# Kernel tuning notes

Hardware: AMD Instinct MI355X
Metric: run time of the kernel (lower is better)

The kernel has to match this reference:

```python
import jax, jax.numpy as jnp
import numpy as np

N = 10000          # nodes
E_RAND = 320000    # random edges (avg degree 32)
F_IN = 512         # nfeat
HID = 256          # args.hid
HEADS = 8          # args.head
FH = HID // HEADS  # 32 per head
NCLASS = 40
TAU = 0.5
LAMDA = 0.5
K = 2


def setup_inputs() -> dict:
    key = jax.random.key(0)
    ks = jax.random.split(key, 16)
    # edge list: random edges + self-loops (so every dst segment is non-empty)
    src = jnp.concatenate([jax.random.randint(ks[0], (E_RAND,), 0, N), jnp.arange(N)])
    dst = jnp.concatenate([jax.random.randint(ks[1], (E_RAND,), 0, N), jnp.arange(N)])
    s = 0.05  # small init scale keeps exp() in attention/bind_loss stable
    return {
        "x": jax.random.normal(ks[2], (N, F_IN), jnp.float32),
        "src": src, "dst": dst,
        "W0": jax.random.normal(ks[3], (F_IN, HEADS, FH), jnp.float32) * s,
        "a0s": jax.random.normal(ks[4], (HEADS, FH), jnp.float32) * s,
        "a0d": jax.random.normal(ks[5], (HEADS, FH), jnp.float32) * s,
        "W1": jax.random.normal(ks[6], (HID, HEADS, FH), jnp.float32) * s,
        "a1s": jax.random.normal(ks[7], (HEADS, FH), jnp.float32) * s,
        "a1d": jax.random.normal(ks[8], (HEADS, FH), jnp.float32) * s,
        "W2": jax.random.normal(ks[9], (HID, HEADS, FH), jnp.float32) * s,
        "a2s": jax.random.normal(ks[10], (HEADS, FH), jnp.float32) * s,
        "a2d": jax.random.normal(ks[11], (HEADS, FH), jnp.float32) * s,
        "Wout": jax.random.normal(ks[12], (HID, HEADS, NCLASS), jnp.float32) * s,
        "aos": jax.random.normal(ks[13], (HEADS, NCLASS), jnp.float32) * s,
        "aod": jax.random.normal(ks[14], (HEADS, NCLASS), jnp.float32) * s,
    }


def _gat_layer(x, W, a_s, a_d, src, dst):
    """Sparse multi-head GAT layer: gather -> edge softmax -> scatter."""
    n = x.shape[0]
    h = jnp.einsum('nf,fhd->nhd', x, W)              # [N,H,Fh]
    es = jnp.sum(h * a_s, axis=-1)                    # [N,H]
    ed = jnp.sum(h * a_d, axis=-1)                    # [N,H]
    e = jax.nn.leaky_relu(es[src] + ed[dst], 0.2)     # [E,H]
    m = jax.ops.segment_max(e, dst, num_segments=n)   # per-dst max (stable softmax)
    w = jnp.exp(e - m[dst])
    z = jax.ops.segment_sum(w, dst, num_segments=n)
    alpha = w / z[dst]                                # [E,H]
    return jax.ops.segment_sum(alpha[:, :, None] * h[src], dst, num_segments=n)  # [N,H,Fh]


def _bind_loss(z):
    # z1 == z2 == z in the original call site: refl_sim == between_sim
    zn = z / jnp.maximum(jnp.linalg.norm(z, axis=1, keepdims=True), 1e-12)
    S = jnp.exp(jnp.matmul(zn, zn.T) / TAU)           # [N,N]
    d = jnp.diagonal(S)
    off = jnp.sum(S, axis=1) - d                      # masked (off-diagonal) row sum
    CT = -jnp.log(d / (off + off))                    # neg_c2.sum + neg_c3.sum
    return jnp.mean(CT)


def reference(x, src, dst, W0, a0s, a0d, W1, a1s, a1d, W2, a2s, a2d, Wout, aos, aod):
    layers = [(W0, a0s, a0d), (W1, a1s, a1d), (W2, a2s, a2d)]
    last = x
    loss = jnp.float32(0.0)
    for i, (W, as_, ad_) in enumerate(layers):
        cur = jax.nn.elu(_gat_layer(last, W, as_, ad_, src, dst))
        cur = cur.reshape(cur.shape[0], -1)           # concat heads -> [N, HID]
        if i > 0:
            beta = LAMDA / (i + 2)                    # MaskLayer(last, cur, lamda, i+2)
            cur = beta * last + (1.0 - beta) * cur
            if i % K == 0:
                loss = loss + _bind_loss(cur)
        last = cur
    out = _gat_layer(last, Wout, aos, aod, src, dst).mean(axis=1)  # avg heads -> [N,C]
    return (jax.nn.log_softmax(out, axis=1), loss)
```

## Files before the change

### kernel.cpp

```cpp
#include <hip/hip_runtime.h>
#include <hip/hip_bf16.h>
#include <math.h>

#define NN_F_IN   512
#define NN_HID    256
#define NN_HEADS  8
#define NN_FH     32
#define NN_NCLASS 40
#define TAU_F     0.5f
#define LAMDA_F   0.5f

typedef __attribute__((ext_vector_type(8))) short bf16x8;
typedef __attribute__((ext_vector_type(4))) float f32x4;

static __device__ __forceinline__ float lrelu02(float x) { return x >= 0.f ? x : 0.2f * x; }
static __device__ __forceinline__ float elu1(float x)    { return x > 0.f ? x : expm1f(x); }
static __device__ __forceinline__ float b2f(unsigned short u) {
    unsigned int x = ((unsigned int)u) << 16;
    return __uint_as_float(x);
}
static __device__ __forceinline__ unsigned short f2b(float f) {
    __hip_bfloat16 hb = __float2bfloat16(f);
    return *reinterpret_cast<unsigned short*>(&hb);
}

__global__ void prep_kernel(const float* __restrict__ x,
                            const float* __restrict__ W0, const float* __restrict__ W1,
                            const float* __restrict__ W2, const float* __restrict__ Wo,
                            unsigned short* __restrict__ Xb,
                            unsigned short* __restrict__ Wt0, unsigned short* __restrict__ Wt1,
                            unsigned short* __restrict__ Wt2, unsigned short* __restrict__ Wto,
                            int n4X) {
    int i = blockIdx.x * 256 + threadIdx.x;
    if (i < n4X) {
        float4 v = *(const float4*)(x + (size_t)i * 4);
        ushort4 o;
        o.x = f2b(v.x); o.y = f2b(v.y); o.z = f2b(v.z); o.w = f2b(v.w);
        *(ushort4*)(Xb + (size_t)i * 4) = o;
        return;
    }
    i -= n4X;
    if (i < 256 * 512) {
        int np = i >> 9, k = i & 511;
        Wt0[i] = f2b(W0[(size_t)k * 256 + np]);
        return;
    }
    i -= 256 * 512;
    if (i < 256 * 256) {
        int np = i >> 8, k = i & 255;
        Wt1[i] = f2b(W1[(size_t)k * 256 + np]);
        return;
    }
    i -= 256 * 256;
    if (i < 256 * 256) {
        int np = i >> 8, k = i & 255;
        Wt2[i] = f2b(W2[(size_t)k * 256 + np]);
        return;
    }
    i -= 256 * 256;
    if (i < 384 * 256) {
        int np = i >> 8, k = i & 255;
        Wto[i] = f2b(np < 320 ? Wo[(size_t)k * 320 + np] : 0.f);
    }
}

__global__ __launch_bounds__(256) void fc_mfma(const unsigned short* __restrict__ A,
                                               const unsigned short* __restrict__ B,
                                               unsigned short* __restrict__ H,
                                               int M, int K, int ncols, int ldH) {
    int t = threadIdx.x, lane = t & 63, wid = t >> 6;
    int wrow = wid >> 1, wcol = wid & 1;
    int l15 = lane & 15, lg = lane >> 4;
    int mbase = blockIdx.y * 64 + wrow * 32;
    int nbase = blockIdx.x * 64 + wcol * 32;

    const unsigned short* Ap[2];
    const unsigned short* Bp[2];
#pragma unroll
    for (int m = 0; m < 2; ++m) {
        int rr = mbase + m * 16 + l15;
        if (rr > M - 1) rr = M - 1;
        Ap[m] = A + (size_t)rr * K + lg * 8;
        Bp[m] = B + (size_t)(nbase + m * 16 + l15) * K + lg * 8;
    }
    f32x4 acc[2][2];
#pragma unroll
    for (int m = 0; m < 2; ++m)
#pragma unroll
        for (int nn = 0; nn < 2; ++nn)
#pragma unroll
            for (int r = 0; r < 4; ++r) acc[m][nn][r] = 0.f;

    bf16x8 aP[2], bP[2], aQ[2], bQ[2];
#pragma unroll
    for (int m = 0; m < 2; ++m) {
        aP[m] = *(const bf16x8*)(Ap[m]);
        bP[m] = *(const bf16x8*)(Bp[m]);
    }
    int nhalf = K >> 6;
    int kk = 32;
    for (int it = 0; it < nhalf; ++it) {
#pragma unroll
        for (int m = 0; m < 2; ++m) {
            aQ[m] = *(const bf16x8*)(Ap[m] + kk);
            bQ[m] = *(const bf16x8*)(Bp[m] + kk);
        }
#pragma unroll
        for (int m = 0; m < 2; ++m)
#pragma unroll
            for (int nn = 0; nn < 2; ++nn)
                acc[m][nn] = __builtin_amdgcn_mfma_f32_16x16x32_bf16(aP[m], bP[nn], acc[m][nn], 0, 0, 0);
        if (it + 1 < nhalf) {
#pragma unroll
            for (int m = 0; m < 2; ++m) {
                aP[m] = *(const bf16x8*)(Ap[m] + kk + 32);
                bP[m] = *(const bf16x8*)(Bp[m] + kk + 32);
            }
        }
#pragma unroll
        for (int m = 0; m < 2; ++m)
#pragma unroll
            for (int nn = 0; nn < 2; ++nn)
                acc[m][nn] = __builtin_amdgcn_mfma_f32_16x16x32_bf16(aQ[m], bQ[nn], acc[m][nn], 0, 0, 0);
        kk += 64;
    }
#pragma unroll
    for (int m = 0; m < 2; ++m) {
#pragma unroll
        for (int nn = 0; nn < 2; ++nn) {
            int col = nbase + nn * 16 + l15;
            if (col >= ncols) continue;
#pragma unroll
            for (int r = 0; r < 4; ++r) {
                int row = mbase + m * 16 + lg * 4 + r;
                if (row < M) H[(size_t)row * ldH + col] = f2b(acc[m][nn][r]);
            }
        }
    }
}

__global__ void attn_kernel(const unsigned short* __restrict__ Hm, const float* __restrict__ As,
                            const float* __restrict__ Ad, float* __restrict__ es,
                            float* __restrict__ ed, int n, int df) {
    int idx = blockIdx.x * blockDim.x + threadIdx.x;
    if (idx >= n * NN_HEADS) return;
    int nn = idx / NN_HEADS, hh = idx - nn * NN_HEADS;
    const unsigned short* hp = Hm + (size_t)nn * NN_HEADS * df + hh * df;
    const float* ap = As + hh * df;
    const float* bp = Ad + hh * df;
    float s1 = 0.f, s2 = 0.f;
    for (int d = 0; d < df; d += 4) {
        ushort4 hv = *(const ushort4*)(hp + d);
        float4 av = *(const float4*)(ap + d);
        float4 bv = *(const float4*)(bp + d);
        float h0 = b2f(hv.x), h1 = b2f(hv.y), h2 = b2f(hv.z), h3 = b2f(hv.w);
        s1 += h0 * av.x + h1 * av.y + h2 * av.z + h3 * av.w;
        s2 += h0 * bv.x + h1 * bv.y + h2 * bv.z + h3 * bv.w;
    }
    es[idx] = s1;
    ed[idx] = s2;
}

__global__ __launch_bounds__(256) void edge_wz(
    const float* __restrict__ es, const float* __restrict__ ed,
    const int* __restrict__ csr_src, const int* __restrict__ row_start,
    float* __restrict__ wC, float* __restrict__ zinv, int n) {
    int lane = threadIdx.x & 63;
    int nn   = blockIdx.x * 4 + (threadIdx.x >> 6);
    if (nn >= n) return;
    int s0 = row_start[nn], s1 = row_start[nn + 1];
    int h    = lane & 7;
    int slot = lane >> 3;
    float edh = ed[nn * NN_HEADS + h];
    float z = 0.f;
    for (int e = s0 + slot; e < s1; e += 8) {
        int sv = csr_src[e];
        float w = __expf(lrelu02(es[sv * NN_HEADS + h] + edh));
        wC[(size_t)e * NN_HEADS + h] = w;
        z += w;
    }
    z += __shfl_xor(z, 8, 64);
    z += __shfl_xor(z, 16, 64);
    z += __shfl_xor(z, 32, 64);
    if (slot == 0) zinv[nn * NN_HEADS + h] = 1.f / z;
}

__global__ void count_kernel(const int* __restrict__ dst, int* __restrict__ counts, int E) {
    int e = blockIdx.x * blockDim.x + threadIdx.x;
    if (e < E) atomicAdd(&counts[dst[e]], 1);
}

__global__ void scan_kernel(const int* __restrict__ counts, int* __restrict__ row_start,
                            int* __restrict__ cursor, int n) {
    __shared__ int s[1024];
    int t  = threadIdx.x;
    int ch = (n + 1023) / 1024;
    int lo = t * ch;
    int sum = 0;
    for (int j = 0; j < ch; ++j) {
        int i = lo + j;
        if (i < n) sum += counts[i];
    }
    s[t] = sum;
    __syncthreads();
    for (int off = 1; off < 1024; off <<= 1) {
        int v = 0;
        if (t >= off) v = s[t - off];
        __syncthreads();
        s[t] += v;
        __syncthreads();
    }
    int run = (t == 0) ? 0 : s[t - 1];
    for (int j = 0; j < ch; ++j) {
        int i = lo + j;
        if (i < n) {
            row_start[i] = run;
            cursor[i] = run;
            run += counts[i];
        }
    }
    if (t == 1023) row_start[n] = s[1023];
}

__global__ void scatter_kernel(const int* __restrict__ src, const int* __restrict__ dst,
                               int* __restrict__ cursor, int* __restrict__ csr_src, int E) {
    int e = blockIdx.x * blockDim.x + threadIdx.x;
    if (e < E) {
        int d   = dst[e];
        int pos = atomicAdd(&cursor[d], 1);
        csr_src[pos] = src[e];
    }
}

__global__ __launch_bounds__(256) void gather_hidden(
    const unsigned short* __restrict__ Hm, const float* __restrict__ wC,
    const float* __restrict__ zinv, const int* __restrict__ csr_src,
    const int* __restrict__ row_start, const unsigned short* __restrict__ last,
    unsigned short* __restrict__ out, int n, float beta) {
    int lane = threadIdx.x & 63;
    int nn   = blockIdx.x * 4 + (threadIdx.x >> 6);
    if (nn >= n) return;
    int s0 = row_start[nn], s1 = row_start[nn + 1];
    int h2 = lane >> 3;

    float a0 = 0.f, a1 = 0.f, a2 = 0.f, a3 = 0.f;
    int fullEnd = s0 + ((s1 - s0) & ~7);
    int e = s0;
    for (; e < fullEnd; e += 8) {
        int idx[8];
        float wv[8];
#pragma unroll
        for (int j = 0; j < 8; ++j) {
            idx[j] = csr_src[e + j];
            wv[j]  = wC[(size_t)(e + j) * NN_HEADS + h2];
        }
        ushort4 r[8];
#pragma unroll
        for (int j = 0; j < 8; ++j) r[j] = *(const ushort4*)&Hm[(size_t)idx[j] * NN_HID + lane * 4];
#pragma unroll
        for (int j = 0; j < 8; ++j) {
            float w = wv[j];
            a0 += w * b2f(r[j].x); a1 += w * b2f(r[j].y);
            a2 += w * b2f(r[j].z); a3 += w * b2f(r[j].w);
        }
    }
    if (e < s1) {
        int c = s1 - e;
        int idx[8];
        float wv[8];
#pragma unroll
        for (int j = 0; j < 8; ++j) {
            int p = (j < c) ? e + j : e;
            idx[j] = csr_src[p];
            wv[j]  = wC[(size_t)p * NN_HEADS + h2];
        }
        ushort4 r[8];
#pragma unroll
        for (int j = 0; j < 8; ++j) r[j] = *(const ushort4*)&Hm[(size_t)idx[j] * NN_HID + lane * 4];
#pragma unroll
        for (int j = 0; j < 8; ++j) {
            if (j < c) {
                float w = wv[j];
                a0 += w * b2f(r[j].x); a1 += w * b2f(r[j].y);
                a2 += w * b2f(r[j].z); a3 += w * b2f(r[j].w);
            }
        }
    }
    float zi = zinv[nn * NN_HEADS + h2];
    float v0 = elu1(a0 * zi), v1 = elu1(a1 * zi), v2 = elu1(a2 * zi), v3 = elu1(a3 * zi);
    if (beta >= 0.f) {
        ushort4 lv = *(const ushort4*)&last[(size_t)nn * NN_HID + lane * 4];
        v0 = beta * b2f(lv.x) + (1.f - beta) * v0;
        v1 = beta * b2f(lv.y) + (1.f - beta) * v1;
        v2 = beta * b2f(lv.z) + (1.f - beta) * v2;
        v3 = beta * b2f(lv.w) + (1.f - beta) * v3;
    }
    ushort4 o;
    o.x = f2b(v0); o.y = f2b(v1); o.z = f2b(v2); o.w = f2b(v3);
    *(ushort4*)&out[(size_t)nn * NN_HID + lane * 4] = o;
}

__global__ void gather_final(const unsigned short* __restrict__ Hm, const float* __restrict__ wC,
                             const float* __restrict__ zinv, const int* __restrict__ csr_src,
                             const int* __restrict__ row_start, float* __restrict__ dout, int n) {
    int nn = blockIdx.x;
    __shared__ float accs[NN_HEADS * NN_NCLASS];
    int t = threadIdx.x;
    int s0 = row_start[nn], s1 = row_start[nn + 1];
    int hh = t / NN_NCLASS;
    float acc = 0.f;
    const int LD = NN_HEADS * NN_NCLASS;
    int fullEnd = s0 + ((s1 - s0) & ~7);
    int e = s0;
    for (; e < fullEnd; e += 8) {
        int idx[8];
        float wv[8];
#pragma unroll
        for (int j = 0; j < 8; ++j) {
            idx[j] = csr_src[e + j];
            wv[j]  = wC[(size_t)(e + j) * NN_HEADS + hh];
        }
        float v[8];
#pragma unroll
        for (int j = 0; j < 8; ++j) v[j] = b2f(Hm[(size_t)idx[j] * LD + t]);
#pragma unroll
        for (int j = 0; j < 8; ++j) acc += wv[j] * v[j];
    }
    if (e < s1) {
        int c = s1 - e;
        int idx[8];
        float wv[8];
#pragma unroll
        for (int j = 0; j < 8; ++j) {
            int p = (j < c) ? e + j : e;
            idx[j] = csr_src[p];
            wv[j]  = wC[(size_t)p * NN_HEADS + hh];
        }
        float v[8];
#pragma unroll
        for (int j = 0; j < 8; ++j) v[j] = b2f(Hm[(size_t)idx[j] * LD + t]);
#pragma unroll
        for (int j = 0; j < 8; ++j) {
            if (j < c) acc += wv[j] * v[j];
        }
    }
    accs[t] = acc * zinv[nn * NN_HEADS + hh];
    __syncthreads();
    if (t < 64) {
        float v = -INFINITY;
        if (t < NN_NCLASS) {
            float sacc = 0.f;
#pragma unroll
            for (int h2 = 0; h2 < NN_HEADS; ++h2) sacc += accs[h2 * NN_NCLASS + t];
            v = sacc * (1.f / NN_HEADS);
        }
        float mx = v;
#pragma unroll
        for (int o = 1; o < 64; o <<= 1) mx = fmaxf(mx, __shfl_xor(mx, o, 64));
        float ex = (t < NN_NCLASS) ? expf(v - mx) : 0.f;
        float se = ex;
#pragma unroll
        for (int o = 1; o < 64; o <<= 1) se += __shfl_xor(se, o, 64);
        if (t < NN_NCLASS) dout[(size_t)nn * NN_NCLASS + t] = (v - mx) - logf(se);
    }
}

__global__ void rownorm_kernel(const unsigned short* __restrict__ z, short* __restrict__ znb,
                               float* __restrict__ dvec, int n) {
    int nn = blockIdx.x;
    int t  = threadIdx.x;
    float v  = b2f(z[(size_t)nn * NN_HID + t]);
    float sq = v * v;
#pragma unroll
    for (int o = 1; o < 64; o <<= 1) sq += __shfl_xor(sq, o, 64);
    __shared__ float ws[4];
    if ((t & 63) == 0) ws[t >> 6] = sq;
    __syncthreads();
    float s = ws[0] + ws[1] + ws[2] + ws[3];
    float m = fmaxf(sqrtf(s), 1e-12f);
    znb[(size_t)nn * NN_HID + t] = (short)f2b(v / m);
    if (t == 0) dvec[nn] = __expf((s / (m * m)) * (1.f / TAU_F));
}

__global__ __launch_bounds__(256) void gram_mfma(const short* __restrict__ znb,
                                                 float* __restrict__ P2d, int n,
                                                 int T, int nwg, int Npad) {
    __shared__ short As[2][128 * 64];
    __shared__ short Bs[2][128 * 64];

    int b = blockIdx.x;
    int q = nwg >> 3, r8 = nwg & 7, xc = b & 7, oo = b >> 3;
    int sid = (xc < r8 ? xc * (q + 1) : r8 * (q + 1) + (xc - r8) * q) + oo;
    int bi = 0, rem = sid;
    while (rem >= T - bi) { rem -= T - bi; ++bi; }
    int bj = bi + rem;
    int i0 = bi * 128, j0 = bj * 128;

    int t    = threadIdx.x;
    int lane = t & 63;
    int wid  = t >> 6;
    int wrow = wid >> 1, wcol = wid & 1;
    int l15  = lane & 15, lg = lane >> 4;
    int srow = lane >> 3;
    int sch  = lane & 7;

    f32x4 acc[4][4];
#pragma unroll
    for (int m = 0; m < 4; ++m)
#pragma unroll
        for (int nn = 0; nn < 4; ++nn)
#pragma unroll
            for (int r = 0; r < 4; ++r) acc[m][nn][r] = 0.f;

    bf16x8 sa[2][4], sb[2][4];
#pragma unroll
    for (int sl = 0; sl < 2; ++sl)
#pragma unroll
        for (int s = 0; s < 4; ++s) {
            int row = wid * 32 + s * 8 + srow;
            int gch = sch ^ (row & 7);
            sa[sl][s] = *(const bf16x8*)(znb + (size_t)(i0 + row) * NN_HID + sl * 64 + gch * 8);
            sb[sl][s] = *(const bf16x8*)(znb + (size_t)(j0 + row) * NN_HID + sl * 64 + gch * 8);
        }

#pragma unroll
    for (int kt = 0; kt < 2; ++kt) {
#pragma unroll
        for (int sl = 0; sl < 2; ++sl)
#pragma unroll
            for (int s = 0; s < 4; ++s) {
                int row = wid * 32 + s * 8 + srow;
                *(bf16x8*)(&As[sl][row * 64 + sch * 8]) = sa[sl][s];
                *(bf16x8*)(&Bs[sl][row * 64 + sch * 8]) = sb[sl][s];
            }
        __syncthreads();
        if (kt == 0) {
#pragma unroll
            for (int sl = 0; sl < 2; ++sl)
#pragma unroll
                for (int s = 0; s < 4; ++s) {
                    int row = wid * 32 + s * 8 + srow;
                    int gch = sch ^ (row & 7);
                    sa[sl][s] = *(const bf16x8*)(znb + (size_t)(i0 + row) * NN_HID + 128 + sl * 64 + gch * 8);
                    sb[sl][s] = *(const bf16x8*)(znb + (size_t)(j0 + row) * NN_HID + 128 + sl * 64 + gch * 8);
                }
        }
#pragma unroll
        for (int sl = 0; sl < 2; ++sl) {
#pragma unroll
            for (int ks = 0; ks < 2; ++ks) {
                bf16x8 av[4], bv[4];
#pragma unroll
                for (int m = 0; m < 4; ++m) {
                    int Ra = wrow * 64 + m * 16 + l15;
                    int Rb = wcol * 64 + m * 16 + l15;
                    int ca = (ks * 4 + lg) ^ (Ra & 7);
                    int cb = (ks * 4 + lg) ^ (Rb & 7);
                    av[m] = *(const bf16x8*)(&As[sl][Ra * 64 + ca * 8]);
                    bv[m] = *(const bf16x8*)(&Bs[sl][Rb * 64 + cb * 8]);
                }
#pragma unroll
                for (int m = 0; m < 4; ++m)
#pragma unroll
                    for (int nn = 0; nn < 4; ++nn)
                        acc[m][nn] = __builtin_amdgcn_mfma_f32_16x16x32_bf16(av[m], bv[nn], acc[m][nn], 0, 0, 0);
            }
        }
        if (kt == 0) __syncthreads();
    }

    int i0w = i0 + wrow * 64;
    int j0w = j0 + wcol * 64;
    bool diag = (bj == bi);
#pragma unroll
    for (int m = 0; m < 4; ++m)
#pragma unroll
        for (int nn = 0; nn < 4; ++nn) {
            int gj = j0w + nn * 16 + l15;
            bool jok = gj < n;
#pragma unroll
            for (int r = 0; r < 4; ++r) {
                int gi = i0w + m * 16 + lg * 4 + r;
                acc[m][nn][r] = (jok && gi < n) ? __expf(acc[m][nn][r] * (1.f / TAU_F)) : 0.f;
            }
        }
    float* rowslot = P2d + (size_t)(2 * bj + wcol) * Npad;
#pragma unroll
    for (int m = 0; m < 4; ++m) {
#pragma unroll
        for (int r = 0; r < 4; ++r) {
            float v = acc[m][0][r] + acc[m][1][r] + acc[m][2][r] + acc[m][3][r];
            v += __shfl_xor(v, 1, 64);
            v += __shfl_xor(v, 2, 64);
            v += __shfl_xor(v, 4, 64);
            v += __shfl_xor(v, 8, 64);
            if (l15 == 0) {
                int gi = i0w + m * 16 + lg * 4 + r;
                if (gi < n) rowslot[gi] = v;
            }
        }
    }
    if (!diag) {
        float* colslot = P2d + (size_t)(2 * bi + wrow) * Npad;
#pragma unroll
        for (int nn = 0; nn < 4; ++nn) {
            float v = 0.f;
#pragma unroll
            for (int m = 0; m < 4; ++m)
#pragma unroll
                for (int r = 0; r < 4; ++r) v += acc[m][nn][r];
            v += __shfl_xor(v, 16, 64);
            v += __shfl_xor(v, 32, 64);
            if (lg == 0) {
                int gj = j0w + nn * 16 + l15;
                if (gj < n) colslot[gj] = v;
            }
        }
    }
}

__global__ void fold_kernel(const float* __restrict__ P2d, float* __restrict__ R,
                            int n, int slots, int Npad) {
    int i = blockIdx.x * 256 + threadIdx.x;
    if (i >= n) return;
    const float* p = P2d + i;
    float s0 = 0.f, s1 = 0.f, s2 = 0.f, s3 = 0.f;
    int sl = 0;
    for (; sl + 4 <= slots; sl += 4) {
        s0 += p[(size_t)(sl + 0) * Npad];
        s1 += p[(size_t)(sl + 1) * Npad];
        s2 += p[(size_t)(sl + 2) * Npad];
        s3 += p[(size_t)(sl + 3) * Npad];
    }
    for (; sl < slots; ++sl) s0 += p[(size_t)sl * Npad];
    R[i] = (s0 + s1) + (s2 + s3);
}

__global__ void loss_kernel(const float* __restrict__ R, const float* __restrict__ dvec,
                            float* __restrict__ out_loss, int n) {
    __shared__ float s[1024];
    int t = threadIdx.x;
    float sum = 0.f;
    for (int i = t; i < n; i += 1024) {
        float d   = dvec[i];
        float off = R[i] - d;
        sum += -logf(d / (off + off));
    }
    s[t] = sum;
    __syncthreads();
    for (int o = 512; o > 0; o >>= 1) {
        if (t < o) s[t] += s[t + o];
        __syncthreads();
    }
    if (t == 0) *out_loss = s[0] / n;
}

extern "C" void kernel_launch(void* const* d_in, const int* in_sizes, int n_in,
                              void* d_out, int out_size, void* d_ws, size_t ws_size,
                              hipStream_t stream) {
    const float* x   = (const float*)d_in[0];
    const int*   src = (const int*)d_in[1];
    const int*   dst = (const int*)d_in[2];
    const float* W0  = (const float*)d_in[3];
    const float* a0s = (const float*)d_in[4];
    const float* a0d = (const float*)d_in[5];
    const float* W1  = (const float*)d_in[6];
    const float* a1s = (const float*)d_in[7];
    const float* a1d = (const float*)d_in[8];
    const float* W2  = (const float*)d_in[9];
    const float* a2s = (const float*)d_in[10];
    const float* a2d = (const float*)d_in[11];
    const float* Wout= (const float*)d_in[12];
    const float* aos = (const float*)d_in[13];
    const float* aod = (const float*)d_in[14];

    int N = in_sizes[0] / NN_F_IN;
    int E = in_sizes[1];
    int Npad = ((N + 127) / 128) * 128;
    int T = Npad / 128;
    int nwg = T * (T + 1) / 2;
    float* out = (float*)d_out;

    char*  ws  = (char*)d_ws;
    size_t off = 0;
    auto alloc = [&](size_t bytes) -> void* {
        void* p = ws + off;
        off += bytes;
        off = (off + 255) & ~(size_t)255;
        return p;
    };
    size_t hbBytes = (size_t)N * 320 * 2;
    size_t znBytes = (size_t)Npad * NN_HID * 2;
    unsigned short* Hb = (unsigned short*)alloc(hbBytes > znBytes ? hbBytes : znBytes);
    short* znb = (short*)Hb;
    unsigned short* Bl = (unsigned short*)alloc((size_t)N * NN_HID * 2);
    unsigned short* Bc = (unsigned short*)alloc((size_t)N * NN_HID * 2);
    size_t xbBytes = (size_t)N * NN_F_IN * 2;
    size_t p2Bytes = (size_t)2 * T * Npad * 4;
    void* XbP2d = alloc(xbBytes > p2Bytes ? xbBytes : p2Bytes);
    unsigned short* Xb  = (unsigned short*)XbP2d;
    float*          P2d = (float*)XbP2d;
    unsigned short* Wt0 = (unsigned short*)alloc((size_t)256 * 512 * 2);
    unsigned short* Wt1 = (unsigned short*)alloc((size_t)256 * 256 * 2);
    unsigned short* Wt2 = (unsigned short*)alloc((size_t)256 * 256 * 2);
    unsigned short* Wto = (unsigned short*)alloc((size_t)384 * 256 * 2);
    float* es     = (float*)alloc((size_t)N * NN_HEADS * 4);
    float* ed     = (float*)alloc((size_t)N * NN_HEADS * 4);
    float* wC     = (float*)alloc((size_t)E * NN_HEADS * 4);
    float* zinvA  = (float*)alloc((size_t)N * NN_HEADS * 4);
    float* Rrow   = (float*)alloc((size_t)N * 4);
    float* dvec   = (float*)alloc((size_t)N * 4);
    int*   counts = (int*)alloc((size_t)N * 4);
    int*   rs     = (int*)alloc((size_t)(N + 1) * 4);
    int*   cursor = (int*)alloc((size_t)N * 4);
    int*   csr    = (int*)alloc((size_t)E * 4);

    hipMemsetAsync(counts, 0, (size_t)N * 4, stream);
    count_kernel<<<(E + 255) / 256, 256, 0, stream>>>(dst, counts, E);
    scan_kernel<<<1, 1024, 0, stream>>>(counts, rs, cursor, N);
    scatter_kernel<<<(E + 255) / 256, 256, 0, stream>>>(src, dst, cursor, csr, E);

    int n4X = N * NN_F_IN / 4;
    int prepTotal = n4X + 256 * 512 + 256 * 256 + 256 * 256 + 384 * 256;
    prep_kernel<<<(prepTotal + 255) / 256, 256, 0, stream>>>(
        x, W0, W1, W2, Wout, Xb, Wt0, Wt1, Wt2, Wto, n4X);

    int atGrid = (N * NN_HEADS + 255) / 256;
    int ghGrid = (N + 3) / 4;
    int mT64 = (N + 63) / 64;

    fc_mfma<<<dim3(4, mT64), 256, 0, stream>>>(Xb, Wt0, Hb, N, 512, 256, 256);
    attn_kernel<<<atGrid, 256, 0, stream>>>(Hb, a0s, a0d, es, ed, N, NN_FH);
    edge_wz<<<ghGrid, 256, 0, stream>>>(es, ed, csr, rs, wC, zinvA, N);
    gather_hidden<<<ghGrid, 256, 0, stream>>>(Hb, wC, zinvA, csr, rs, nullptr, Bl, N, -1.f);

    fc_mfma<<<dim3(4, mT64), 256, 0, stream>>>(Bl, Wt1, Hb, N, 256, 256, 256);
    attn_kernel<<<atGrid, 256, 0, stream>>>(Hb, a1s, a1d, es, ed, N, NN_FH);
    edge_wz<<<ghGrid, 256, 0, stream>>>(es, ed, csr, rs, wC, zinvA, N);
    gather_hidden<<<ghGrid, 256, 0, stream>>>(Hb, wC, zinvA, csr, rs, Bl, Bc, N, LAMDA_F / 3.f);

    fc_mfma<<<dim3(4, mT64), 256, 0, stream>>>(Bc, Wt2, Hb, N, 256, 256, 256);
    attn_kernel<<<atGrid, 256, 0, stream>>>(Hb, a2s, a2d, es, ed, N, NN_FH);
    edge_wz<<<ghGrid, 256, 0, stream>>>(es, ed, csr, rs, wC, zinvA, N);
    gather_hidden<<<ghGrid, 256, 0, stream>>>(Hb, wC, zinvA, csr, rs, Bc, Bl, N, LAMDA_F / 4.f);

    rownorm_kernel<<<N, 256, 0, stream>>>(Bl, znb, dvec, N);
    hipMemsetAsync(znb + (size_t)N * NN_HID, 0, (size_t)(Npad - N) * NN_HID * 2, stream);
    hipMemsetAsync(P2d, 0, (size_t)2 * T * Npad * 4, stream);
    gram_mfma<<<nwg, 256, 0, stream>>>(znb, P2d, N, T, nwg, Npad);
    fold_kernel<<<(N + 255) / 256, 256, 0, stream>>>(P2d, Rrow, N, 2 * T, Npad);
    loss_kernel<<<1, 1024, 0, stream>>>(Rrow, dvec, out + (size_t)N * NN_NCLASS, N);

    fc_mfma<<<dim3(5, mT64), 256, 0, stream>>>(Bl, Wto, Hb, N, 256, 320, 320);
    attn_kernel<<<atGrid, 256, 0, stream>>>(Hb, aos, aod, es, ed, N, NN_NCLASS);
    edge_wz<<<ghGrid, 256, 0, stream>>>(es, ed, csr, rs, wC, zinvA, N);
    gather_final<<<N, NN_HEADS * NN_NCLASS, 0, stream>>>(Hb, wC, zinvA, csr, rs, out, N);
}
```

Measured before the change: 408.8 us.

## Rework Gram kernel to 8 waves, fold exp scale into bf16 rows, drop memsets

```diff
diff --git a/kernel.cpp b/kernel.cpp
--- a/kernel.cpp
+++ b/kernel.cpp
@@ -9,6 +9,7 @@
 #define NN_NCLASS 40
 #define TAU_F     0.5f
 #define LAMDA_F   0.5f
+#define ZN_SCALE  1.6986436f
 
 typedef __attribute__((ext_vector_type(8))) short bf16x8;
 typedef __attribute__((ext_vector_type(4))) float f32x4;
@@ -369,6 +370,10 @@
                                float* __restrict__ dvec, int n) {
     int nn = blockIdx.x;
     int t  = threadIdx.x;
+    if (nn >= n) {
+        znb[(size_t)nn * NN_HID + t] = 0;
+        return;
+    }
     float v  = b2f(z[(size_t)nn * NN_HID + t]);
     float sq = v * v;
 #pragma unroll
@@ -378,11 +383,11 @@
     __syncthreads();
     float s = ws[0] + ws[1] + ws[2] + ws[3];
     float m = fmaxf(sqrtf(s), 1e-12f);
-    znb[(size_t)nn * NN_HID + t] = (short)f2b(v / m);
+    znb[(size_t)nn * NN_HID + t] = (short)f2b((v / m) * ZN_SCALE);
     if (t == 0) dvec[nn] = __expf((s / (m * m)) * (1.f / TAU_F));
 }
 
-__global__ __launch_bounds__(256) void gram_mfma(const short* __restrict__ znb,
+__global__ __launch_bounds__(512) void gram_mfma(const short* __restrict__ znb,
                                                  float* __restrict__ P2d, int n,
                                                  int T, int nwg, int Npad) {
     __shared__ short As[2][128 * 64];
@@ -399,25 +404,25 @@
     int t    = threadIdx.x;
     int lane = t & 63;
     int wid  = t >> 6;
-    int wrow = wid >> 1, wcol = wid & 1;
+    int wrow = wid >> 2, wcol = wid & 3;
     int l15  = lane & 15, lg = lane >> 4;
     int srow = lane >> 3;
     int sch  = lane & 7;
 
-    f32x4 acc[4][4];
+    f32x4 acc[4][2];
 #pragma unroll
     for (int m = 0; m < 4; ++m)
 #pragma unroll
-        for (int nn = 0; nn < 4; ++nn)
+        for (int nn = 0; nn < 2; ++nn)
 #pragma unroll
             for (int r = 0; r < 4; ++r) acc[m][nn][r] = 0.f;
 
-    bf16x8 sa[2][4], sb[2][4];
+    bf16x8 sa[2][2], sb[2][2];
 #pragma unroll
     for (int sl = 0; sl < 2; ++sl)
 #pragma unroll
-        for (int s = 0; s < 4; ++s) {
-            int row = wid * 32 + s * 8 + srow;
+        for (int s = 0; s < 2; ++s) {
+            int row = wid * 16 + s * 8 + srow;
             int gch = sch ^ (row & 7);
             sa[sl][s] = *(const bf16x8*)(znb + (size_t)(i0 + row) * NN_HID + sl * 64 + gch * 8);
             sb[sl][s] = *(const bf16x8*)(znb + (size_t)(j0 + row) * NN_HID + sl * 64 + gch * 8);
@@ -428,8 +433,8 @@
 #pragma unroll
         for (int sl = 0; sl < 2; ++sl)
 #pragma unroll
-            for (int s = 0; s < 4; ++s) {
-                int row = wid * 32 + s * 8 + srow;
+            for (int s = 0; s < 2; ++s) {
+                int row = wid * 16 + s * 8 + srow;
                 *(bf16x8*)(&As[sl][row * 64 + sch * 8]) = sa[sl][s];
                 *(bf16x8*)(&Bs[sl][row * 64 + sch * 8]) = sb[sl][s];
             }
@@ -438,8 +443,8 @@
 #pragma unroll
             for (int sl = 0; sl < 2; ++sl)
 #pragma unroll
-                for (int s = 0; s < 4; ++s) {
-                    int row = wid * 32 + s * 8 + srow;
+                for (int s = 0; s < 2; ++s) {
+                    int row = wid * 16 + s * 8 + srow;
                     int gch = sch ^ (row & 7);
                     sa[sl][s] = *(const bf16x8*)(znb + (size_t)(i0 + row) * NN_HID + 128 + sl * 64 + gch * 8);
                     sb[sl][s] = *(const bf16x8*)(znb + (size_t)(j0 + row) * NN_HID + 128 + sl * 64 + gch * 8);
@@ -449,20 +454,23 @@
         for (int sl = 0; sl < 2; ++sl) {
 #pragma unroll
             for (int ks = 0; ks < 2; ++ks) {
-                bf16x8 av[4], bv[4];
+                bf16x8 av[4], bv[2];
 #pragma unroll
                 for (int m = 0; m < 4; ++m) {
                     int Ra = wrow * 64 + m * 16 + l15;
-                    int Rb = wcol * 64 + m * 16 + l15;
                     int ca = (ks * 4 + lg) ^ (Ra & 7);
+                    av[m] = *(const bf16x8*)(&As[sl][Ra * 64 + ca * 8]);
+                }
+#pragma unroll
+                for (int nn = 0; nn < 2; ++nn) {
+                    int Rb = wcol * 32 + nn * 16 + l15;
                     int cb = (ks * 4 + lg) ^ (Rb & 7);
-                    av[m] = *(const bf16x8*)(&As[sl][Ra * 64 + ca * 8]);
-                    bv[m] = *(const bf16x8*)(&Bs[sl][Rb * 64 + cb * 8]);
+                    bv[nn] = *(const bf16x8*)(&Bs[sl][Rb * 64 + cb * 8]);
                 }
 #pragma unroll
                 for (int m = 0; m < 4; ++m)
 #pragma unroll
-                    for (int nn = 0; nn < 4; ++nn)
+                    for (int nn = 0; nn < 2; ++nn)
                         acc[m][nn] = __builtin_amdgcn_mfma_f32_16x16x32_bf16(av[m], bv[nn], acc[m][nn], 0, 0, 0);
             }
         }
@@ -470,26 +478,36 @@
     }
 
     int i0w = i0 + wrow * 64;
-    int j0w = j0 + wcol * 64;
+    int j0w = j0 + wcol * 32;
     bool diag = (bj == bi);
-#pragma unroll
-    for (int m = 0; m < 4; ++m)
-#pragma unroll
-        for (int nn = 0; nn < 4; ++nn) {
-            int gj = j0w + nn * 16 + l15;
-            bool jok = gj < n;
-#pragma unroll
-            for (int r = 0; r < 4; ++r) {
-                int gi = i0w + m * 16 + lg * 4 + r;
-                acc[m][nn][r] = (jok && gi < n) ? __expf(acc[m][nn][r] * (1.f / TAU_F)) : 0.f;
-            }
-        }
-    float* rowslot = P2d + (size_t)(2 * bj + wcol) * Npad;
+    if (bj == T - 1) {
+#pragma unroll
+        for (int m = 0; m < 4; ++m)
+#pragma unroll
+            for (int nn = 0; nn < 2; ++nn) {
+                int gj = j0w + nn * 16 + l15;
+                bool jok = gj < n;
+#pragma unroll
+                for (int r = 0; r < 4; ++r) {
+                    int gi = i0w + m * 16 + lg * 4 + r;
+                    acc[m][nn][r] = (jok && gi < n) ? __builtin_exp2f(acc[m][nn][r]) : 0.f;
+                }
+            }
+    } else {
+#pragma unroll
+        for (int m = 0; m < 4; ++m)
+#pragma unroll
+            for (int nn = 0; nn < 2; ++nn)
+#pragma unroll
+                for (int r = 0; r < 4; ++r)
+                    acc[m][nn][r] = __builtin_exp2f(acc[m][nn][r]);
+    }
+    float* rowslot = P2d + (size_t)(4 * bj + wcol) * Npad;
 #pragma unroll
     for (int m = 0; m < 4; ++m) {
 #pragma unroll
         for (int r = 0; r < 4; ++r) {
-            float v = acc[m][0][r] + acc[m][1][r] + acc[m][2][r] + acc[m][3][r];
+            float v = acc[m][0][r] + acc[m][1][r];
             v += __shfl_xor(v, 1, 64);
             v += __shfl_xor(v, 2, 64);
             v += __shfl_xor(v, 4, 64);
@@ -501,9 +519,9 @@
         }
     }
     if (!diag) {
-        float* colslot = P2d + (size_t)(2 * bi + wrow) * Npad;
-#pragma unroll
-        for (int nn = 0; nn < 4; ++nn) {
+        float* colslot = P2d + (size_t)(4 * T + 2 * bi + wrow) * Npad;
+#pragma unroll
+        for (int nn = 0; nn < 2; ++nn) {
             float v = 0.f;
 #pragma unroll
             for (int m = 0; m < 4; ++m)
@@ -520,20 +538,21 @@
 }
 
 __global__ void fold_kernel(const float* __restrict__ P2d, float* __restrict__ R,
-                            int n, int slots, int Npad) {
+                            int n, int T, int Npad) {
     int i = blockIdx.x * 256 + threadIdx.x;
     if (i >= n) return;
-    const float* p = P2d + i;
-    float s0 = 0.f, s1 = 0.f, s2 = 0.f, s3 = 0.f;
-    int sl = 0;
-    for (; sl + 4 <= slots; sl += 4) {
-        s0 += p[(size_t)(sl + 0) * Npad];
-        s1 += p[(size_t)(sl + 1) * Npad];
-        s2 += p[(size_t)(sl + 2) * Npad];
-        s3 += p[(size_t)(sl + 3) * Npad];
-    }
-    for (; sl < slots; ++sl) s0 += p[(size_t)sl * Npad];
-    R[i] = (s0 + s1) + (s2 + s3);
+    int p = i >> 7;
+    const float* base = P2d + i;
+    float s = 0.f;
+    for (int bj = p; bj < T; ++bj) {
+        const float* qq = base + (size_t)(4 * bj) * Npad;
+        s += qq[0] + qq[(size_t)Npad] + qq[(size_t)2 * Npad] + qq[(size_t)3 * Npad];
+    }
+    const float* c0 = base + (size_t)(4 * T) * Npad;
+    for (int bi = 0; bi < p; ++bi) {
+        s += c0[(size_t)(2 * bi) * Npad] + c0[(size_t)(2 * bi + 1) * Npad];
+    }
+    R[i] = s;
 }
 
 __global__ void loss_kernel(const float* __restrict__ R, const float* __restrict__ dvec,
@@ -596,7 +615,7 @@
     unsigned short* Bl = (unsigned short*)alloc((size_t)N * NN_HID * 2);
     unsigned short* Bc = (unsigned short*)alloc((size_t)N * NN_HID * 2);
     size_t xbBytes = (size_t)N * NN_F_IN * 2;
-    size_t p2Bytes = (size_t)2 * T * Npad * 4;
+    size_t p2Bytes = (size_t)6 * T * Npad * 4;
     void* XbP2d = alloc(xbBytes > p2Bytes ? xbBytes : p2Bytes);
     unsigned short* Xb  = (unsigned short*)XbP2d;
     float*          P2d = (float*)XbP2d;
@@ -644,11 +663,9 @@
     edge_wz<<<ghGrid, 256, 0, stream>>>(es, ed, csr, rs, wC, zinvA, N);
     gather_hidden<<<ghGrid, 256, 0, stream>>>(Hb, wC, zinvA, csr, rs, Bc, Bl, N, LAMDA_F / 4.f);
 
-    rownorm_kernel<<<N, 256, 0, stream>>>(Bl, znb, dvec, N);
-    hipMemsetAsync(znb + (size_t)N * NN_HID, 0, (size_t)(Npad - N) * NN_HID * 2, stream);
-    hipMemsetAsync(P2d, 0, (size_t)2 * T * Npad * 4, stream);
-    gram_mfma<<<nwg, 256, 0, stream>>>(znb, P2d, N, T, nwg, Npad);
-    fold_kernel<<<(N + 255) / 256, 256, 0, stream>>>(P2d, Rrow, N, 2 * T, Npad);
+    rownorm_kernel<<<Npad, 256, 0, stream>>>(Bl, znb, dvec, N);
+    gram_mfma<<<nwg, 512, 0, stream>>>(znb, P2d, N, T, nwg, Npad);
+    fold_kernel<<<(N + 255) / 256, 256, 0, stream>>>(P2d, Rrow, N, T, Npad);
     loss_kernel<<<1, 1024, 0, stream>>>(Rrow, dvec, out + (size_t)N * NN_NCLASS, N);
 
     fc_mfma<<<dim3(5, mT64), 256, 0, stream>>>(Bl, Wto, Hb, N, 256, 320, 320);
```

Measured after the change: 418.7 us. 1.02x slower.

## Fuse edge softmax into gather and stream gram tiles via direct LDS loads

Applied to the files above, without the earlier changes.

```diff
diff --git a/kernel.cpp b/kernel.cpp
--- a/kernel.cpp
+++ b/kernel.cpp
@@ -9,9 +9,13 @@
 #define NN_NCLASS 40
 #define TAU_F     0.5f
 #define LAMDA_F   0.5f
+#define ZN_SCALE  1.6986436f
 
 typedef __attribute__((ext_vector_type(8))) short bf16x8;
 typedef __attribute__((ext_vector_type(4))) float f32x4;
+
+typedef __attribute__((address_space(1))) unsigned int gu32_t;
+typedef __attribute__((address_space(3))) unsigned int lu32_t;
 
 static __device__ __forceinline__ float lrelu02(float x) { return x >= 0.f ? x : 0.2f * x; }
 static __device__ __forceinline__ float elu1(float x)    { return x > 0.f ? x : expm1f(x); }
@@ -233,8 +237,8 @@
 }
 
 __global__ __launch_bounds__(256) void gather_hidden(
-    const unsigned short* __restrict__ Hm, const float* __restrict__ wC,
-    const float* __restrict__ zinv, const int* __restrict__ csr_src,
+    const unsigned short* __restrict__ Hm, const float* __restrict__ es,
+    const float* __restrict__ ed, const int* __restrict__ csr_src,
     const int* __restrict__ row_start, const unsigned short* __restrict__ last,
     unsigned short* __restrict__ out, int n, float beta) {
     int lane = threadIdx.x & 63;
@@ -242,24 +246,26 @@
     if (nn >= n) return;
     int s0 = row_start[nn], s1 = row_start[nn + 1];
     int h2 = lane >> 3;
-
+    float edh = ed[nn * NN_HEADS + h2];
+
+    float zacc = 0.f;
     float a0 = 0.f, a1 = 0.f, a2 = 0.f, a3 = 0.f;
     int fullEnd = s0 + ((s1 - s0) & ~7);
     int e = s0;
     for (; e < fullEnd; e += 8) {
         int idx[8];
-        float wv[8];
+        float q[8];
+#pragma unroll
+        for (int j = 0; j < 8; ++j) idx[j] = csr_src[e + j];
+#pragma unroll
+        for (int j = 0; j < 8; ++j) q[j] = es[idx[j] * NN_HEADS + h2];
+        ushort4 r[8];
+#pragma unroll
+        for (int j = 0; j < 8; ++j) r[j] = *(const ushort4*)&Hm[(size_t)idx[j] * NN_HID + lane * 4];
 #pragma unroll
         for (int j = 0; j < 8; ++j) {
-            idx[j] = csr_src[e + j];
-            wv[j]  = wC[(size_t)(e + j) * NN_HEADS + h2];
-        }
-        ushort4 r[8];
-#pragma unroll
-        for (int j = 0; j < 8; ++j) r[j] = *(const ushort4*)&Hm[(size_t)idx[j] * NN_HID + lane * 4];
-#pragma unroll
-        for (int j = 0; j < 8; ++j) {
-            float w = wv[j];
+            float w = __expf(lrelu02(q[j] + edh));
+            zacc += w;
             a0 += w * b2f(r[j].x); a1 += w * b2f(r[j].y);
             a2 += w * b2f(r[j].z); a3 += w * b2f(r[j].w);
         }
@@ -267,26 +273,25 @@
     if (e < s1) {
         int c = s1 - e;
         int idx[8];
-        float wv[8];
-#pragma unroll
-        for (int j = 0; j < 8; ++j) {
-            int p = (j < c) ? e + j : e;
-            idx[j] = csr_src[p];
-            wv[j]  = wC[(size_t)p * NN_HEADS + h2];
-        }
+        float q[8];
+#pragma unroll
+        for (int j = 0; j < 8; ++j) idx[j] = csr_src[(j < c) ? e + j : e];
+#pragma unroll
+        for (int j = 0; j < 8; ++j) q[j] = es[idx[j] * NN_HEADS + h2];
         ushort4 r[8];
 #pragma unroll
         for (int j = 0; j < 8; ++j) r[j] = *(const ushort4*)&Hm[(size_t)idx[j] * NN_HID + lane * 4];
 #pragma unroll
         for (int j = 0; j < 8; ++j) {
             if (j < c) {
-                float w = wv[j];
+                float w = __expf(lrelu02(q[j] + edh));
+                zacc += w;
                 a0 += w * b2f(r[j].x); a1 += w * b2f(r[j].y);
                 a2 += w * b2f(r[j].z); a3 += w * b2f(r[j].w);
             }
         }
     }
-    float zi = zinv[nn * NN_HEADS + h2];
+    float zi = 1.f / zacc;
     float v0 = elu1(a0 * zi), v1 = elu1(a1 * zi), v2 = elu1(a2 * zi), v3 = elu1(a3 * zi);
     if (beta >= 0.f) {
         ushort4 lv = *(const ushort4*)&last[(size_t)nn * NN_HID + lane * 4];
@@ -369,6 +374,10 @@
                                float* __restrict__ dvec, int n) {
     int nn = blockIdx.x;
     int t  = threadIdx.x;
+    if (nn >= n) {
+        znb[(size_t)nn * NN_HID + t] = 0;
+        return;
+    }
     float v  = b2f(z[(size_t)nn * NN_HID + t]);
     float sq = v * v;
 #pragma unroll
@@ -378,15 +387,15 @@
     __syncthreads();
     float s = ws[0] + ws[1] + ws[2] + ws[3];
     float m = fmaxf(sqrtf(s), 1e-12f);
-    znb[(size_t)nn * NN_HID + t] = (short)f2b(v / m);
+    znb[(size_t)nn * NN_HID + t] = (short)f2b((v / m) * ZN_SCALE);
     if (t == 0) dvec[nn] = __expf((s / (m * m)) * (1.f / TAU_F));
 }
 
 __global__ __launch_bounds__(256) void gram_mfma(const short* __restrict__ znb,
                                                  float* __restrict__ P2d, int n,
                                                  int T, int nwg, int Npad) {
-    __shared__ short As[2][128 * 64];
-    __shared__ short Bs[2][128 * 64];
+    __shared__ short As[128 * 32];
+    __shared__ short Bs[128 * 32];
 
     int b = blockIdx.x;
     int q = nwg >> 3, r8 = nwg & 7, xc = b & 7, oo = b >> 3;
@@ -401,8 +410,20 @@
     int wid  = t >> 6;
     int wrow = wid >> 1, wcol = wid & 1;
     int l15  = lane & 15, lg = lane >> 4;
-    int srow = lane >> 3;
-    int sch  = lane & 7;
+
+    int srow0 = 16 * (2 * wid + 0) + (lane >> 2);
+    int srow1 = 16 * (2 * wid + 1) + (lane >> 2);
+    int kc    = lane & 3;
+    int kc0   = kc ^ ((srow0 >> 1) & 3);
+    int kc1   = kc ^ ((srow1 >> 1) & 3);
+    const short* gA0 = znb + (size_t)(i0 + srow0) * NN_HID + kc0 * 8;
+    const short* gA1 = znb + (size_t)(i0 + srow1) * NN_HID + kc1 * 8;
+    const short* gB0 = znb + (size_t)(j0 + srow0) * NN_HID + kc0 * 8;
+    const short* gB1 = znb + (size_t)(j0 + srow1) * NN_HID + kc1 * 8;
+    short* lA0 = As + (2 * wid + 0) * 512 + lane * 8;
+    short* lA1 = As + (2 * wid + 1) * 512 + lane * 8;
+    short* lB0 = Bs + (2 * wid + 0) * 512 + lane * 8;
+    short* lB1 = Bs + (2 * wid + 1) * 512 + lane * 8;
 
     f32x4 acc[4][4];
 #pragma unroll
@@ -412,78 +433,60 @@
 #pragma unroll
             for (int r = 0; r < 4; ++r) acc[m][nn][r] = 0.f;
 
-    bf16x8 sa[2][4], sb[2][4];
-#pragma unroll
-    for (int sl = 0; sl < 2; ++sl)
-#pragma unroll
-        for (int s = 0; s < 4; ++s) {
-            int row = wid * 32 + s * 8 + srow;
-            int gch = sch ^ (row & 7);
-            sa[sl][s] = *(const bf16x8*)(znb + (size_t)(i0 + row) * NN_HID + sl * 64 + gch * 8);
-            sb[sl][s] = *(const bf16x8*)(znb + (size_t)(j0 + row) * NN_HID + sl * 64 + gch * 8);
-        }
-
-#pragma unroll
-    for (int kt = 0; kt < 2; ++kt) {
-#pragma unroll
-        for (int sl = 0; sl < 2; ++sl)
-#pragma unroll
-            for (int s = 0; s < 4; ++s) {
-                int row = wid * 32 + s * 8 + srow;
-                *(bf16x8*)(&As[sl][row * 64 + sch * 8]) = sa[sl][s];
-                *(bf16x8*)(&Bs[sl][row * 64 + sch * 8]) = sb[sl][s];
-            }
+#pragma unroll
+    for (int s = 0; s < 8; ++s) {
+        int ko = s * 32;
+        __builtin_amdgcn_global_load_lds((gu32_t*)(gA0 + ko), (lu32_t*)lA0, 16, 0, 0);
+        __builtin_amdgcn_global_load_lds((gu32_t*)(gA1 + ko), (lu32_t*)lA1, 16, 0, 0);
+        __builtin_amdgcn_global_load_lds((gu32_t*)(gB0 + ko), (lu32_t*)lB0, 16, 0, 0);
+        __builtin_amdgcn_global_load_lds((gu32_t*)(gB1 + ko), (lu32_t*)lB1, 16, 0, 0);
         __syncthreads();
-        if (kt == 0) {
-#pragma unroll
-            for (int sl = 0; sl < 2; ++sl)
-#pragma unroll
-                for (int s = 0; s < 4; ++s) {
-                    int row = wid * 32 + s * 8 + srow;
-                    int gch = sch ^ (row & 7);
-                    sa[sl][s] = *(const bf16x8*)(znb + (size_t)(i0 + row) * NN_HID + 128 + sl * 64 + gch * 8);
-                    sb[sl][s] = *(const bf16x8*)(znb + (size_t)(j0 + row) * NN_HID + 128 + sl * 64 + gch * 8);
-                }
-        }
-#pragma unroll
-        for (int sl = 0; sl < 2; ++sl) {
-#pragma unroll
-            for (int ks = 0; ks < 2; ++ks) {
-                bf16x8 av[4], bv[4];
-#pragma unroll
-                for (int m = 0; m < 4; ++m) {
-                    int Ra = wrow * 64 + m * 16 + l15;
-                    int Rb = wcol * 64 + m * 16 + l15;
-                    int ca = (ks * 4 + lg) ^ (Ra & 7);
-                    int cb = (ks * 4 + lg) ^ (Rb & 7);
-                    av[m] = *(const bf16x8*)(&As[sl][Ra * 64 + ca * 8]);
-                    bv[m] = *(const bf16x8*)(&Bs[sl][Rb * 64 + cb * 8]);
-                }
-#pragma unroll
-                for (int m = 0; m < 4; ++m)
-#pragma unroll
-                    for (int nn = 0; nn < 4; ++nn)
-                        acc[m][nn] = __builtin_amdgcn_mfma_f32_16x16x32_bf16(av[m], bv[nn], acc[m][nn], 0, 0, 0);
-            }
-        }
-        if (kt == 0) __syncthreads();
+        bf16x8 av[4], bv[4];
+#pragma unroll
+        for (int m = 0; m < 4; ++m) {
+            int Ra = wrow * 64 + m * 16 + l15;
+            int ca = lg ^ ((Ra >> 1) & 3);
+            av[m] = *(const bf16x8*)&As[Ra * 32 + ca * 8];
+        }
+#pragma unroll
+        for (int m = 0; m < 4; ++m) {
+            int Rb = wcol * 64 + m * 16 + l15;
+            int cb = lg ^ ((Rb >> 1) & 3);
+            bv[m] = *(const bf16x8*)&Bs[Rb * 32 + cb * 8];
+        }
+#pragma unroll
+        for (int m = 0; m < 4; ++m)
+#pragma unroll
+            for (int nn = 0; nn < 4; ++nn)
+                acc[m][nn] = __builtin_amdgcn_mfma_f32_16x16x32_bf16(av[m], bv[nn], acc[m][nn], 0, 0, 0);
+        __syncthreads();
     }
 
     int i0w = i0 + wrow * 64;
     int j0w = j0 + wcol * 64;
     bool diag = (bj == bi);
-#pragma unroll
-    for (int m = 0; m < 4; ++m)
-#pragma unroll
-        for (int nn = 0; nn < 4; ++nn) {
-            int gj = j0w + nn * 16 + l15;
-            bool jok = gj < n;
-#pragma unroll
-            for (int r = 0; r < 4; ++r) {
-                int gi = i0w + m * 16 + lg * 4 + r;
-                acc[m][nn][r] = (jok && gi < n) ? __expf(acc[m][nn][r] * (1.f / TAU_F)) : 0.f;
+    if (bj == T - 1) {
+#pragma unroll
+        for (int m = 0; m < 4; ++m)
+#pragma unroll
+            for (int nn = 0; nn < 4; ++nn) {
+                int gj = j0w + nn * 16 + l15;
+                bool jok = gj < n;
+#pragma unroll
+                for (int r = 0; r < 4; ++r) {
+                    int gi = i0w + m * 16 + lg * 4 + r;
+                    acc[m][nn][r] = (jok && gi < n) ? __builtin_exp2f(acc[m][nn][r]) : 0.f;
+                }
             }
-        }
+    } else {
+#pragma unroll
+        for (int m = 0; m < 4; ++m)
+#pragma unroll
+            for (int nn = 0; nn < 4; ++nn)
+#pragma unroll
+                for (int r = 0; r < 4; ++r)
+                    acc[m][nn][r] = __builtin_exp2f(acc[m][nn][r]);
+    }
     float* rowslot = P2d + (size_t)(2 * bj + wcol) * Npad;
 #pragma unroll
     for (int m = 0; m < 4; ++m) {
@@ -631,22 +634,17 @@
 
     fc_mfma<<<dim3(4, mT64), 256, 0, stream>>>(Xb, Wt0, Hb, N, 512, 256, 256);
     attn_kernel<<<atGrid, 256, 0, stream>>>(Hb, a0s, a0d, es, ed, N, NN_FH);
-    edge_wz<<<ghGrid, 256, 0, stream>>>(es, ed, csr, rs, wC, zinvA, N);
-    gather_hidden<<<ghGrid, 256, 0, stream>>>(Hb, wC, zinvA, csr, rs, nullptr, Bl, N, -1.f);
+    gather_hidden<<<ghGrid, 256, 0, stream>>>(Hb, es, ed, csr, rs, nullptr, Bl, N, -1.f);
 
     fc_mfma<<<dim3(4, mT64), 256, 0, stream>>>(Bl, Wt1, Hb, N, 256, 256, 256);
     attn_kernel<<<atGrid, 256, 0, stream>>>(Hb, a1s, a1d, es, ed, N, NN_FH);
-    edge_wz<<<ghGrid, 256, 0, stream>>>(es, ed, csr, rs, wC, zinvA, N);
-    gather_hidden<<<ghGrid, 256, 0, stream>>>(Hb, wC, zinvA, csr, rs, Bl, Bc, N, LAMDA_F / 3.f);
+    gather_hidden<<<ghGrid, 256, 0, stream>>>(Hb, es, ed, csr, rs, Bl, Bc, N, LAMDA_F / 3.f);
 
     fc_mfma<<<dim3(4, mT64), 256, 0, stream>>>(Bc, Wt2, Hb, N, 256, 256, 256);
     attn_kernel<<<atGrid, 256, 0, stream>>>(Hb, a2s, a2d, es, ed, N, NN_FH);
-    edge_wz<<<ghGrid, 256, 0, stream>>>(es, ed, csr, rs, wC, zinvA, N);
-    gather_hidden<<<ghGrid, 256, 0, stream>>>(Hb, wC, zinvA, csr, rs, Bc, Bl, N, LAMDA_F / 4.f);
-
-    rownorm_kernel<<<N, 256, 0, stream>>>(Bl, znb, dvec, N);
-    hipMemsetAsync(znb + (size_t)N * NN_HID, 0, (size_t)(Npad - N) * NN_HID * 2, stream);
-    hipMemsetAsync(P2d, 0, (size_t)2 * T * Npad * 4, stream);
+    gather_hidden<<<ghGrid, 256, 0, stream>>>(Hb, es, ed, csr, rs, Bc, Bl, N, LAMDA_F / 4.f);
+
+    rownorm_kernel<<<Npad, 256, 0, stream>>>(Bl, znb, dvec, N);
     gram_mfma<<<nwg, 256, 0, stream>>>(znb, P2d, N, T, nwg, Npad);
     fold_kernel<<<(N + 255) / 256, 256, 0, stream>>>(P2d, Rrow, N, 2 * T, Npad);
     loss_kernel<<<1, 1024, 0, stream>>>(Rrow, dvec, out + (size_t)N * NN_NCLASS, N);
```

Result: faster. 384.8 us (-5.9%).
